# Performance work log

Measured on AMD Instinct MI355X. Metric: run time of the kernel, lower is better.

## Reference

```python
import jax, jax.numpy as jnp
import numpy as np

DIM, HEADS, WH, WW, MLAT, MLON = 512, 8, 8, 8, 32, 64
N = WH * WW
B = MLAT * MLON
PER_LAT = (2 * WH - 1) * (2 * WW - 1)  # 225


def _make_rel_idx():
    # Swin 2D relative position index inside one window
    ch, cw = np.arange(WH), np.arange(WW)
    coords = np.stack(np.meshgrid(ch, cw, indexing='ij')).reshape(2, -1)  # (2, N)
    rel = coords[:, :, None] - coords[:, None, :]                          # (2, N, N)
    rel = rel.transpose(1, 2, 0).astype(np.int64)
    rel[..., 0] += WH - 1
    rel[..., 1] += WW - 1
    rel[..., 0] *= 2 * WW - 1
    idx2d = rel.sum(-1)                                                    # (N, N)
    # earth-specific: each lat row i gets its own 225-entry slab; lon diff is 0
    idx = idx2d[None] + np.arange(MLAT)[:, None, None] * PER_LAT           # (Mlat, N, N)
    idx = np.broadcast_to(idx[:, None], (MLAT, MLON, N, N)).reshape(B, N, N)
    return jnp.asarray(idx.astype(np.int32))


def setup_inputs() -> dict:
    key = jax.random.key(0)
    k = jax.random.split(key, 5)
    x = jax.random.normal(k[0], (B, N, DIM), dtype=jnp.float32)
    w_qkv = jax.random.normal(k[1], (3 * DIM, DIM), dtype=jnp.float32) * 0.02
    b_qkv = jnp.zeros((3 * DIM,), dtype=jnp.float32)
    w_proj = jax.random.normal(k[2], (DIM, DIM), dtype=jnp.float32) * 0.02
    b_proj = jnp.zeros((DIM,), dtype=jnp.float32)
    bias_table = jax.random.normal(k[3], (MLAT * PER_LAT, HEADS), dtype=jnp.float32) * 0.02
    return {
        'x': x, 'w_qkv': w_qkv, 'b_qkv': b_qkv,
        'w_proj': w_proj, 'b_proj': b_proj,
        'bias_table': bias_table, 'rel_idx': _make_rel_idx(),
    }


def reference(x, w_qkv, b_qkv, w_proj, b_proj, bias_table, rel_idx):
    Bn, Nn, C = x.shape
    D = C // HEADS
    qkv = (x @ w_qkv.T + b_qkv).reshape(Bn, Nn, 3, HEADS, D)
    q = jnp.transpose(qkv[:, :, 0], (0, 2, 1, 3))  # (B, H, N, D)
    k = jnp.transpose(qkv[:, :, 1], (0, 2, 1, 3))
    v = jnp.transpose(qkv[:, :, 2], (0, 2, 1, 3))
    # gather learned earth bias: (B, N, N, H) -> (B, H, N, N)
    bias = jnp.transpose(bias_table[rel_idx], (0, 3, 1, 2))
    scale = D ** -0.5  # SDPA default scale (qk_scale is None)
    attn = jax.nn.softmax(jnp.einsum('bhnd,bhmd->bhnm', q, k) * scale + bias, axis=-1)
    out = jnp.einsum('bhnm,bhmd->bhnd', attn, v)
    out = jnp.transpose(out, (0, 2, 1, 3)).reshape(Bn, Nn, C)
    return out @ w_proj.T + b_proj
```

## Files before the change

### kernel.cpp

```cpp
#include <hip/hip_runtime.h>
#include <stdint.h>

typedef __attribute__((ext_vector_type(8))) short short8;
typedef __attribute__((ext_vector_type(4))) short short4v;
typedef __attribute__((ext_vector_type(4))) float float4v;

__device__ __forceinline__ short f2bf(float f) {
  uint32_t u = __builtin_bit_cast(uint32_t, f);
  u += 0x7FFFu + ((u >> 16) & 1u);
  return (short)(u >> 16);
}

__device__ __forceinline__ void gl_lds16(const short* g, short* l) {
  __builtin_amdgcn_global_load_lds(
      (const __attribute__((address_space(1))) unsigned int*)g,
      (__attribute__((address_space(3))) unsigned int*)l, 16, 0, 0);
}


__global__ void prep_weights(const float* __restrict__ wq, const float* __restrict__ wp,
                             short* __restrict__ wq_b, short* __restrict__ wp_b) {
  int i = blockIdx.x * blockDim.x + threadIdx.x;
  int stride = gridDim.x * blockDim.x;
  for (int j = i; j < 786432 / 4; j += stride) {
    float4 v = ((const float4*)wq)[j];
    short4v t = {f2bf(v.x), f2bf(v.y), f2bf(v.z), f2bf(v.w)};
    ((short4v*)wq_b)[j] = t;
  }
  for (int j = i; j < 262144 / 4; j += stride) {
    float4 v = ((const float4*)wp)[j];
    short4v t = {f2bf(v.x), f2bf(v.y), f2bf(v.z), f2bf(v.w)};
    ((short4v*)wp_b)[j] = t;
  }
}

__global__ __launch_bounds__(1024, 4)
void qkv_attn(const float* __restrict__ x, const short* __restrict__ wq,
              const float* __restrict__ bqkv, const float* __restrict__ btab,
              short* __restrict__ attn) {
  __shared__ short Xs[64 * 512];
  __shared__ short Qs[4][64 * 64];
  __shared__ short Ks[4][64 * 64];
  __shared__ short Vt[4][64 * 64];

  const int blk  = blockIdx.x;
  const int tid  = threadIdx.x;
  const int lane = tid & 63;
  const int w    = tid >> 6;
  const int l16  = lane & 15;
  const int quad = lane >> 4;
  const int r    = l16 & 7;
  const int offE = ((quad ^ (r & 3)) << 3) | ((r >> 2) << 5);
  const int offO = offE ^ 32;

  const int g  = w >> 2;
  const int st = w & 3;

#pragma unroll 1
  for (int vi = 0; vi < 4; ++vi) {
    const int b   = blk * 4 + vi;
    const int lat = b >> 6;

    const float* xw = x + (size_t)b * (64 * 512);
    for (int c = tid; c < 64 * 128; c += 1024) {
      int n = c >> 7, kc = c & 127;
      float4 v = *(const float4*)(xw + n * 512 + kc * 4);
      short4v t = {f2bf(v.x), f2bf(v.y), f2bf(v.z), f2bf(v.w)};
      *(short4v*)&Xs[n * 512 + ((kc * 4) ^ ((n & 7) << 3))] = t;
    }
    __syncthreads();

#pragma unroll 1
    for (int h0 = 0; h0 < 8; h0 += 4) {
      {
        const int hq = h0 + g;
        const int hk = h0 + (g ^ 1);
        const short* Aq = wq + (size_t)((hq * 64 + st * 16 + l16) * 512) + quad * 8;
        const short* Ak = wq + (size_t)((512 + hk * 64 + st * 16 + l16) * 512) + quad * 8;
        const short* Av = wq + (size_t)((1024 + hq * 64 + st * 16 + l16) * 512) + quad * 8;
        const short* xE = &Xs[l16 * 512 + offE];
        const short* xO = &Xs[l16 * 512 + offO];

        short8 wqp[3], wkp[3], wvp[3];
        wqp[0] = *(const short8*)(Aq);      wqp[1] = *(const short8*)(Aq + 32);
        wkp[0] = *(const short8*)(Ak);      wkp[1] = *(const short8*)(Ak + 32);
        wvp[0] = *(const short8*)(Av);      wvp[1] = *(const short8*)(Av + 32);

        float4v aQ[4] = {}, aK[4] = {}, aV[4] = {};
#pragma unroll
        for (int j = 0; j < 16; ++j) {
          if (j + 2 < 16) {
            wqp[(j + 2) % 3] = *(const short8*)(Aq + (j + 2) * 32);
            wkp[(j + 2) % 3] = *(const short8*)(Ak + (j + 2) * 32);
            wvp[(j + 2) % 3] = *(const short8*)(Av + (j + 2) * 32);
          }
          const short* xb = (j & 1) ? xO : xE;
          const int xoff = (j >> 1) * 64;
          short8 x0 = *(const short8*)(xb + xoff);
          short8 x1 = *(const short8*)(xb + 8192 + xoff);
          short8 x2 = *(const short8*)(xb + 16384 + xoff);
          short8 x3 = *(const short8*)(xb + 24576 + xoff);
          short8 Wq = wqp[j % 3], Wk = wkp[j % 3], Wv = wvp[j % 3];
          aQ[0] = __builtin_amdgcn_mfma_f32_16x16x32_bf16(Wq, x0, aQ[0], 0, 0, 0);
          aQ[1] = __builtin_amdgcn_mfma_f32_16x16x32_bf16(Wq, x1, aQ[1], 0, 0, 0);
          aQ[2] = __builtin_amdgcn_mfma_f32_16x16x32_bf16(Wq, x2, aQ[2], 0, 0, 0);
          aQ[3] = __builtin_amdgcn_mfma_f32_16x16x32_bf16(Wq, x3, aQ[3], 0, 0, 0);
          aK[0] = __builtin_amdgcn_mfma_f32_16x16x32_bf16(Wk, x0, aK[0], 0, 0, 0);
          aK[1] = __builtin_amdgcn_mfma_f32_16x16x32_bf16(Wk, x1, aK[1], 0, 0, 0);
          aK[2] = __builtin_amdgcn_mfma_f32_16x16x32_bf16(Wk, x2, aK[2], 0, 0, 0);
          aK[3] = __builtin_amdgcn_mfma_f32_16x16x32_bf16(Wk, x3, aK[3], 0, 0, 0);
          aV[0] = __builtin_amdgcn_mfma_f32_16x16x32_bf16(x0, Wv, aV[0], 0, 0, 0);
          aV[1] = __builtin_amdgcn_mfma_f32_16x16x32_bf16(x1, Wv, aV[1], 0, 0, 0);
          aV[2] = __builtin_amdgcn_mfma_f32_16x16x32_bf16(x2, Wv, aV[2], 0, 0, 0);
          aV[3] = __builtin_amdgcn_mfma_f32_16x16x32_bf16(x3, Wv, aV[3], 0, 0, 0);
        }

        float bq[4], bk[4];
#pragma unroll
        for (int i = 0; i < 4; ++i) {
          bq[i] = bqkv[hq * 64 + st * 16 + quad * 4 + i];
          bk[i] = bqkv[512 + hk * 64 + st * 16 + quad * 4 + i];
        }
        short* dq = &Qs[g][0];
        short* dk = &Ks[g ^ 1][0];
        const int swqk = (st * 16 + quad * 4) ^ (r << 3);
#pragma unroll
        for (int t = 0; t < 4; ++t) {
          int n = t * 16 + l16;
          short4v pq, pk;
#pragma unroll
          for (int i = 0; i < 4; ++i) {
            pq[i] = f2bf((aQ[t][i] + bq[i]) * 0.125f);
            pk[i] = f2bf(aK[t][i] + bk[i]);
          }
          *(short4v*)&dq[n * 64 + swqk] = pq;
          *(short4v*)&dk[n * 64 + swqk] = pk;
        }
        float bv = bqkv[1024 + hq * 64 + st * 16 + l16];
        const int dv = st * 16 + l16;
#pragma unroll
        for (int t = 0; t < 4; ++t) {
          short4v pv;
#pragma unroll
          for (int i = 0; i < 4; ++i) pv[i] = f2bf(aV[t][i] + bv);
          *(short4v*)&Vt[g][dv * 64 + ((t * 16 + quad * 4) ^ (r << 3))] = pv;
        }
      }
      __syncthreads();

      {
        const int hsel = w >> 2;
        const int h    = h0 + hsel;
        const int n0   = (w & 3) * 16;
        const short* Qb = &Qs[hsel][0];
        const short* Kb = &Ks[hsel][0];
        const short* Vb = &Vt[hsel][0];

        float4v s4[4] = {};
#pragma unroll
        for (int j = 0; j < 2; ++j) {
          const int o = j ? offO : offE;
          short8 a = *(const short8*)&Qb[(n0 + l16) * 64 + o];
#pragma unroll
          for (int t = 0; t < 4; ++t) {
            short8 bf = *(const short8*)&Kb[(t * 16 + l16) * 64 + o];
            s4[t] = __builtin_amdgcn_mfma_f32_16x16x32_bf16(a, bf, s4[t], 0, 0, 0);
          }
        }
#pragma unroll
        for (int t = 0; t < 4; ++t) {
          int m = t * 16 + l16;
#pragma unroll
          for (int i = 0; i < 4; ++i) {
            int n = n0 + quad * 4 + i;
            int idx = ((n >> 3) - (m >> 3) + 7) * 15 + ((n & 7) - (m & 7) + 7) + lat * 225;
            s4[t][i] += btab[idx * 8 + h];
          }
        }
        float p[4][4];
#pragma unroll
        for (int i = 0; i < 4; ++i) {
          float mx = fmaxf(fmaxf(s4[0][i], s4[1][i]), fmaxf(s4[2][i], s4[3][i]));
          mx = fmaxf(mx, __shfl_xor(mx, 1));
          mx = fmaxf(mx, __shfl_xor(mx, 2));
          mx = fmaxf(mx, __shfl_xor(mx, 4));
          mx = fmaxf(mx, __shfl_xor(mx, 8));
          float e0 = __expf(s4[0][i] - mx), e1 = __expf(s4[1][i] - mx);
          float e2 = __expf(s4[2][i] - mx), e3 = __expf(s4[3][i] - mx);
          float sm = e0 + e1 + e2 + e3;
          sm += __shfl_xor(sm, 1);
          sm += __shfl_xor(sm, 2);
          sm += __shfl_xor(sm, 4);
          sm += __shfl_xor(sm, 8);
          float inv = 1.0f / sm;
          p[0][i] = e0 * inv; p[1][i] = e1 * inv; p[2][i] = e2 * inv; p[3][i] = e3 * inv;
        }
        short* Pw = &Qs[hsel][0];
#pragma unroll
        for (int t = 0; t < 4; ++t)
#pragma unroll
          for (int i = 0; i < 4; ++i) {
            int row = n0 + quad * 4 + i;
            Pw[row * 64 + ((t * 16 + l16) ^ ((row & 7) << 3))] = f2bf(p[t][i]);
          }

        float4v o4[4] = {};
#pragma unroll
        for (int j = 0; j < 2; ++j) {
          const int o = j ? offO : offE;
          short8 a = *(const short8*)&Qb[(n0 + l16) * 64 + o];
#pragma unroll
          for (int t = 0; t < 4; ++t) {
            short8 bf = *(const short8*)&Vb[(t * 16 + l16) * 64 + o];
            o4[t] = __builtin_amdgcn_mfma_f32_16x16x32_bf16(a, bf, o4[t], 0, 0, 0);
          }
        }
        short* ob = attn + (size_t)b * (64 * 512);
#pragma unroll
        for (int t = 0; t < 4; ++t)
#pragma unroll
          for (int i = 0; i < 4; ++i)
            ob[(n0 + quad * 4 + i) * 512 + h * 64 + t * 16 + l16] = f2bf(o4[t][i]);
      }
      __syncthreads();
    }
  }
}

__device__ __forceinline__ void stage_tile(const short* __restrict__ ga,
                                           const short* __restrict__ gb,
                                           short* lA, short* lB,
                                           int w, int srow, int scol) {
#pragma unroll
  for (int j = 0; j < 2; ++j) {
    int c = w * 2 + j;
    gl_lds16(ga + (size_t)(c * 8 + srow) * 512 + scol, &lA[c * 512]);
    gl_lds16(gb + (size_t)(c * 8 + srow) * 512 + scol, &lB[c * 512]);
  }
}

__device__ __forceinline__ void compute_tile(const short* As_, const short* Bs_,
                                             float4v (&acc)[2][4],
                                             int wm, int wn, int l16,
                                             int offE, int offO) {
#pragma unroll
  for (int ks = 0; ks < 2; ++ks) {
    const int o = ks ? offO : offE;
    short8 a[2], bf[4];
#pragma unroll
    for (int ti = 0; ti < 2; ++ti)
      a[ti] = *(const short8*)&As_[(wm * 32 + ti * 16 + l16) * 64 + o];
#pragma unroll
    for (int tj = 0; tj < 4; ++tj)
      bf[tj] = *(const short8*)&Bs_[(wn * 64 + tj * 16 + l16) * 64 + o];
#pragma unroll
    for (int ti = 0; ti < 2; ++ti)
#pragma unroll
      for (int tj = 0; tj < 4; ++tj)
        acc[ti][tj] = __builtin_amdgcn_mfma_f32_16x16x32_bf16(a[ti], bf[tj], acc[ti][tj], 0, 0, 0);
  }
}

__global__ __launch_bounds__(512, 4)
void proj_gemm(const short* __restrict__ attn, const short* __restrict__ wp,
               const float* __restrict__ bproj, float* __restrict__ out) {
  __shared__ short As0[128 * 64];
  __shared__ short As1[128 * 64];
  __shared__ short Bs0[128 * 64];
  __shared__ short Bs1[128 * 64];

  const int orig = blockIdx.x;
  const int wg   = (orig & 7) * 128 + (orig >> 3);
  const int n0   = (wg & 3) * 128;
  const int mp   = wg >> 2;

  const int tid  = threadIdx.x;
  const int lane = tid & 63;
  const int w    = tid >> 6;
  const int l16  = lane & 15;
  const int quad = lane >> 4;
  const int wm   = w >> 1, wn = w & 1;
  const int r    = l16 & 7;
  const int offE = ((quad ^ (r & 3)) << 3) | ((r >> 2) << 5);
  const int offO = offE ^ 32;

  const int srow = lane >> 3;
  const int scol = ((lane & 7) ^ srow) * 8;

  const short* gB = wp + (size_t)n0 * 512;

  float bj[4];
#pragma unroll
  for (int tj = 0; tj < 4; ++tj) bj[tj] = bproj[n0 + wn * 64 + tj * 16 + l16];

#pragma unroll 1
  for (int it = 0; it < 4; ++it) {
    const int m0 = mp * 512 + it * 128;
    const short* gA = attn + (size_t)m0 * 512;

    float4v acc[2][4] = {};

    stage_tile(gA, gB, As0, Bs0, w, srow, scol);
    __syncthreads();
#pragma unroll
    for (int kt = 0; kt < 8; kt += 2) {
      if (kt + 1 < 8) stage_tile(gA + (kt + 1) * 64, gB + (kt + 1) * 64, As1, Bs1, w, srow, scol);
      compute_tile(As0, Bs0, acc, wm, wn, l16, offE, offO);
      __syncthreads();
      if (kt + 2 < 8) stage_tile(gA + (kt + 2) * 64, gB + (kt + 2) * 64, As0, Bs0, w, srow, scol);
      compute_tile(As1, Bs1, acc, wm, wn, l16, offE, offO);
      __syncthreads();
    }

#pragma unroll
    for (int ti = 0; ti < 2; ++ti)
#pragma unroll
      for (int i = 0; i < 4; ++i) {
        size_t rowoff = (size_t)(m0 + wm * 32 + ti * 16 + quad * 4 + i) * 512;
#pragma unroll
        for (int tj = 0; tj < 4; ++tj)
          out[rowoff + n0 + wn * 64 + tj * 16 + l16] = acc[ti][tj][i] + bj[tj];
      }
  }
}

extern "C" void kernel_launch(void* const* d_in, const int* in_sizes, int n_in,
                              void* d_out, int out_size, void* d_ws, size_t ws_size,
                              hipStream_t stream) {
  const float* x     = (const float*)d_in[0];
  const float* wqkv  = (const float*)d_in[1];
  const float* bqkv  = (const float*)d_in[2];
  const float* wproj = (const float*)d_in[3];
  const float* bproj = (const float*)d_in[4];
  const float* btab  = (const float*)d_in[5];
  float* out = (float*)d_out;

  short* wq_b = (short*)d_ws;
  short* wp_b = wq_b + 786432;
  short* attn = wp_b + 262144;

  prep_weights<<<256, 256, 0, stream>>>(wqkv, wproj, wq_b, wp_b);
  qkv_attn<<<512, 1024, 0, stream>>>(x, wq_b, bqkv, btab, attn);
  proj_gemm<<<1024, 512, 0, stream>>>(attn, wp_b, bproj, out);
}
```

Baseline: 1.045 ms.

## Fuse output projection GEMM into the QKV attention kernel

Drops the separate projection GEMM kernel and the bf16 attention intermediate in global memory. Each block stores the per-head attention output for four heads into LDS, reusing the Ks buffer, then accumulates the projection into per-wave registers with W_proj fragments read straight from global memory. The bias is added and fp32 results are written once per window. This saves a kernel launch and a global round trip of the intermediate, at the cost of extra barriers, more register pressure (8 accumulators plus 8 bias values) and uncached W_proj loads from global memory in every block.

```diff
diff --git a/kernel.cpp b/kernel.cpp
--- a/kernel.cpp
+++ b/kernel.cpp
@@ -9,12 +9,6 @@
   uint32_t u = __builtin_bit_cast(uint32_t, f);
   u += 0x7FFFu + ((u >> 16) & 1u);
   return (short)(u >> 16);
-}
-
-__device__ __forceinline__ void gl_lds16(const short* g, short* l) {
-  __builtin_amdgcn_global_load_lds(
-      (const __attribute__((address_space(1))) unsigned int*)g,
-      (__attribute__((address_space(3))) unsigned int*)l, 16, 0, 0);
 }
 
 
@@ -35,13 +29,16 @@
 }
 
 __global__ __launch_bounds__(1024, 4)
-void qkv_attn(const float* __restrict__ x, const short* __restrict__ wq,
-              const float* __restrict__ bqkv, const float* __restrict__ btab,
-              short* __restrict__ attn) {
+void qkv_attn_proj(const float* __restrict__ x, const short* __restrict__ wq,
+                   const float* __restrict__ bqkv, const float* __restrict__ btab,
+                   const short* __restrict__ wp, const float* __restrict__ bproj,
+                   float* __restrict__ out) {
   __shared__ short Xs[64 * 512];
   __shared__ short Qs[4][64 * 64];
   __shared__ short Ks[4][64 * 64];
   __shared__ short Vt[4][64 * 64];
+
+  short* Os = &Ks[0][0];
 
   const int blk  = blockIdx.x;
   const int tid  = threadIdx.x;
@@ -55,11 +52,19 @@
 
   const int g  = w >> 2;
   const int st = w & 3;
+  const int cs = w & 3;
+  const int cg = w >> 2;
+
+  float bj[8];
+#pragma unroll
+  for (int tj = 0; tj < 8; ++tj) bj[tj] = bproj[cg * 128 + tj * 16 + l16];
 
 #pragma unroll 1
   for (int vi = 0; vi < 4; ++vi) {
     const int b   = blk * 4 + vi;
     const int lat = b >> 6;
+
+    float4v pacc[8] = {};
 
     const float* xw = x + (size_t)b * (64 * 512);
     for (int c = tid; c < 64 * 128; c += 1024) {
@@ -148,14 +153,15 @@
       }
       __syncthreads();
 
-      {
-        const int hsel = w >> 2;
-        const int h    = h0 + hsel;
-        const int n0   = (w & 3) * 16;
-        const short* Qb = &Qs[hsel][0];
-        const short* Kb = &Ks[hsel][0];
-        const short* Vb = &Vt[hsel][0];
-
+      const int hsel = w >> 2;
+      const int h    = h0 + hsel;
+      const int n0   = (w & 3) * 16;
+      const short* Qb = &Qs[hsel][0];
+      const short* Kb = &Ks[hsel][0];
+      const short* Vb = &Vt[hsel][0];
+
+      float p[4][4];
+      {
         float4v s4[4] = {};
 #pragma unroll
         for (int j = 0; j < 2; ++j) {
@@ -177,7 +183,6 @@
             s4[t][i] += btab[idx * 8 + h];
           }
         }
-        float p[4][4];
 #pragma unroll
         for (int i = 0; i < 4; ++i) {
           float mx = fmaxf(fmaxf(s4[0][i], s4[1][i]), fmaxf(s4[2][i], s4[3][i]));
@@ -195,6 +200,10 @@
           float inv = 1.0f / sm;
           p[0][i] = e0 * inv; p[1][i] = e1 * inv; p[2][i] = e2 * inv; p[3][i] = e3 * inv;
         }
+      }
+      __syncthreads();
+
+      {
         short* Pw = &Qs[hsel][0];
 #pragma unroll
         for (int t = 0; t < 4; ++t)
@@ -215,112 +224,50 @@
             o4[t] = __builtin_amdgcn_mfma_f32_16x16x32_bf16(a, bf, o4[t], 0, 0, 0);
           }
         }
-        short* ob = attn + (size_t)b * (64 * 512);
 #pragma unroll
         for (int t = 0; t < 4; ++t)
 #pragma unroll
-          for (int i = 0; i < 4; ++i)
-            ob[(n0 + quad * 4 + i) * 512 + h * 64 + t * 16 + l16] = f2bf(o4[t][i]);
+          for (int i = 0; i < 4; ++i) {
+            int row = n0 + quad * 4 + i;
+            Os[row * 256 + hsel * 64 + ((t * 16 + l16) ^ ((row & 7) << 3))] = f2bf(o4[t][i]);
+          }
+      }
+      __syncthreads();
+
+      {
+        const int kbase = h0 * 64;
+        const short* OsA = Os + (cs * 16 + l16) * 256;
+        const short* wpb = wp + (size_t)(cg * 128 + l16) * 512 + kbase + quad * 8;
+#pragma unroll
+        for (int ks = 0; ks < 8; ++ks) {
+          short8 a = *(const short8*)(OsA + (ks >> 1) * 64 + ((ks & 1) ? offO : offE));
+          short8 wf[4];
+#pragma unroll
+          for (int tj = 0; tj < 4; ++tj)
+            wf[tj] = *(const short8*)(wpb + tj * 8192 + ks * 32);
+#pragma unroll
+          for (int tj = 0; tj < 4; ++tj)
+            pacc[tj] = __builtin_amdgcn_mfma_f32_16x16x32_bf16(a, wf[tj], pacc[tj], 0, 0, 0);
+#pragma unroll
+          for (int tj = 0; tj < 4; ++tj)
+            wf[tj] = *(const short8*)(wpb + (tj + 4) * 8192 + ks * 32);
+#pragma unroll
+          for (int tj = 0; tj < 4; ++tj)
+            pacc[tj + 4] = __builtin_amdgcn_mfma_f32_16x16x32_bf16(a, wf[tj], pacc[tj + 4], 0, 0, 0);
+        }
       }
       __syncthreads();
     }
-  }
-}
-
-__device__ __forceinline__ void stage_tile(const short* __restrict__ ga,
-                                           const short* __restrict__ gb,
-                                           short* lA, short* lB,
-                                           int w, int srow, int scol) {
-#pragma unroll
-  for (int j = 0; j < 2; ++j) {
-    int c = w * 2 + j;
-    gl_lds16(ga + (size_t)(c * 8 + srow) * 512 + scol, &lA[c * 512]);
-    gl_lds16(gb + (size_t)(c * 8 + srow) * 512 + scol, &lB[c * 512]);
-  }
-}
-
-__device__ __forceinline__ void compute_tile(const short* As_, const short* Bs_,
-                                             float4v (&acc)[2][4],
-                                             int wm, int wn, int l16,
-                                             int offE, int offO) {
-#pragma unroll
-  for (int ks = 0; ks < 2; ++ks) {
-    const int o = ks ? offO : offE;
-    short8 a[2], bf[4];
-#pragma unroll
-    for (int ti = 0; ti < 2; ++ti)
-      a[ti] = *(const short8*)&As_[(wm * 32 + ti * 16 + l16) * 64 + o];
-#pragma unroll
-    for (int tj = 0; tj < 4; ++tj)
-      bf[tj] = *(const short8*)&Bs_[(wn * 64 + tj * 16 + l16) * 64 + o];
-#pragma unroll
-    for (int ti = 0; ti < 2; ++ti)
-#pragma unroll
-      for (int tj = 0; tj < 4; ++tj)
-        acc[ti][tj] = __builtin_amdgcn_mfma_f32_16x16x32_bf16(a[ti], bf[tj], acc[ti][tj], 0, 0, 0);
-  }
-}
-
-__global__ __launch_bounds__(512, 4)
-void proj_gemm(const short* __restrict__ attn, const short* __restrict__ wp,
-               const float* __restrict__ bproj, float* __restrict__ out) {
-  __shared__ short As0[128 * 64];
-  __shared__ short As1[128 * 64];
-  __shared__ short Bs0[128 * 64];
-  __shared__ short Bs1[128 * 64];
-
-  const int orig = blockIdx.x;
-  const int wg   = (orig & 7) * 128 + (orig >> 3);
-  const int n0   = (wg & 3) * 128;
-  const int mp   = wg >> 2;
-
-  const int tid  = threadIdx.x;
-  const int lane = tid & 63;
-  const int w    = tid >> 6;
-  const int l16  = lane & 15;
-  const int quad = lane >> 4;
-  const int wm   = w >> 1, wn = w & 1;
-  const int r    = l16 & 7;
-  const int offE = ((quad ^ (r & 3)) << 3) | ((r >> 2) << 5);
-  const int offO = offE ^ 32;
-
-  const int srow = lane >> 3;
-  const int scol = ((lane & 7) ^ srow) * 8;
-
-  const short* gB = wp + (size_t)n0 * 512;
-
-  float bj[4];
-#pragma unroll
-  for (int tj = 0; tj < 4; ++tj) bj[tj] = bproj[n0 + wn * 64 + tj * 16 + l16];
-
-#pragma unroll 1
-  for (int it = 0; it < 4; ++it) {
-    const int m0 = mp * 512 + it * 128;
-    const short* gA = attn + (size_t)m0 * 512;
-
-    float4v acc[2][4] = {};
-
-    stage_tile(gA, gB, As0, Bs0, w, srow, scol);
-    __syncthreads();
-#pragma unroll
-    for (int kt = 0; kt < 8; kt += 2) {
-      if (kt + 1 < 8) stage_tile(gA + (kt + 1) * 64, gB + (kt + 1) * 64, As1, Bs1, w, srow, scol);
-      compute_tile(As0, Bs0, acc, wm, wn, l16, offE, offO);
-      __syncthreads();
-      if (kt + 2 < 8) stage_tile(gA + (kt + 2) * 64, gB + (kt + 2) * 64, As0, Bs0, w, srow, scol);
-      compute_tile(As1, Bs1, acc, wm, wn, l16, offE, offO);
-      __syncthreads();
+
+    {
+      float* ob = out + (size_t)b * (64 * 512);
+#pragma unroll
+      for (int tj = 0; tj < 8; ++tj)
+#pragma unroll
+        for (int i = 0; i < 4; ++i)
+          ob[(size_t)(cs * 16 + quad * 4 + i) * 512 + cg * 128 + tj * 16 + l16] =
+              pacc[tj][i] + bj[tj];
     }
-
-#pragma unroll
-    for (int ti = 0; ti < 2; ++ti)
-#pragma unroll
-      for (int i = 0; i < 4; ++i) {
-        size_t rowoff = (size_t)(m0 + wm * 32 + ti * 16 + quad * 4 + i) * 512;
-#pragma unroll
-        for (int tj = 0; tj < 4; ++tj)
-          out[rowoff + n0 + wn * 64 + tj * 16 + l16] = acc[ti][tj][i] + bj[tj];
-      }
   }
 }
 
@@ -337,9 +284,7 @@
 
   short* wq_b = (short*)d_ws;
   short* wp_b = wq_b + 786432;
-  short* attn = wp_b + 262144;
 
   prep_weights<<<256, 256, 0, stream>>>(wqkv, wproj, wq_b, wp_b);
-  qkv_attn<<<512, 1024, 0, stream>>>(x, wq_b, bqkv, btab, attn);
-  proj_gemm<<<1024, 512, 0, stream>>>(attn, wp_b, bproj, out);
-}
+  qkv_attn_proj<<<512, 1024, 0, stream>>>(x, wq_b, bqkv, btab, wp_b, bproj, out);
+}
```

Measured after the change: 1.628 ms. 1.56x slower.
